# Kernel tuning notes

Measured on AMD Instinct MI355X. Metric: run time of the kernel, lower is better.

Reference implementation:

```python
import jax, jax.numpy as jnp
import numpy as np

MAX_SIGMA = 10.0
TRUNCATE = 4.0
R = int(TRUNCATE * MAX_SIGMA + 0.5)  # 40, static max radius (scipy: int(truncate*sigma+0.5))
L = 2 * R + 1                         # 81


def _make_kernels(sigmas):
    # sigmas: [B] -> kernels [B, L], exactly matching scipy._gaussian_kernel1d
    pos = jnp.arange(-R, R + 1, dtype=sigmas.dtype)          # [L]
    r = jnp.floor(TRUNCATE * sigmas + 0.5)                   # per-sample radius
    w = jnp.exp(-0.5 * (pos[None, :] ** 2) / (sigmas[:, None] ** 2))
    w = w * (jnp.abs(pos)[None, :] <= r[:, None])            # scipy truncation
    return w / jnp.sum(w, axis=-1, keepdims=True)


def _reflect_index(n):
    # symmetric ('reflect' in scipy) boundary indices for pad width R, valid even if R > n
    i = jnp.arange(-R, n + R)
    j = jnp.mod(i, 2 * n)
    return jnp.where(j < n, j, 2 * n - 1 - j)


def _conv_last(x, k):
    # correlate along last axis with reflect boundary; x [..., n], k [L]
    n = x.shape[-1]
    xp = x[..., _reflect_index(n)]                            # [..., n+2R]
    flat = xp.reshape(-1, 1, n + 2 * R)
    out = jax.lax.conv_general_dilated(flat, k[None, None, :],
                                       window_strides=(1,), padding='VALID')
    return out.reshape(x.shape)


def _blur_one(xi, k):
    # xi: [C, H, W]; scipy gaussian_filter with scalar sigma blurs every axis
    for ax in range(xi.ndim):
        xi = jnp.moveaxis(_conv_last(jnp.moveaxis(xi, ax, -1), k), -1, ax)
    return xi


def setup_inputs() -> dict:
    key = jax.random.key(0)
    k1, _ = jax.random.split(key)
    B, C, H, W = 64, 3, 512, 512
    x = jax.random.uniform(k1, (B, C, H, W), dtype=jnp.float32)
    blur_sigmas = jnp.asarray(np.geomspace(0.5, MAX_SIGMA, 10), dtype=jnp.float32)
    fwd_steps = jax.random.randint(jax.random.fold_in(key, 1), (B,), 0, 10, dtype=jnp.int32)
    return {"x": x, "blur_sigmas": blur_sigmas, "fwd_steps": fwd_steps}


def reference(x, blur_sigmas, fwd_steps):
    sigmas = blur_sigmas[fwd_steps]          # [B]
    kernels = _make_kernels(sigmas)          # [B, L]
    return jax.vmap(_blur_one)(x, kernels)   # [B, C, H, W]
```

## Files before the change

kernel.cpp:

```cpp
#include <hip/hip_runtime.h>
#include <hip/hip_bf16.h>

#define RMAX 40
#define LK   81
#define HH   512
#define WW   512
#define CC   3
#define BB   64
#define ROWS 2

__global__ void prep_kernel(const float* __restrict__ sigmas10,
                            const int* __restrict__ steps,
                            int* __restrict__ rbuf,
                            float* __restrict__ mbuf,
                            float* __restrict__ wbuf)
{
    int b = threadIdx.x;
    if (b >= BB) return;
    float sigma = sigmas10[steps[b]];
    int r = (int)floorf(4.0f * sigma + 0.5f);
    if (r > RMAX) r = RMAX;
    float s2 = sigma * sigma;

    float sum = 0.0f;
    for (int p = -r; p <= r; ++p)
        sum += expf(-0.5f * (float)(p * p) / s2);
    float inv = 1.0f / sum;

    for (int i = 0; i < 128; ++i) wbuf[b * 128 + i] = 0.0f;
    for (int p = -r; p <= r; ++p)
        wbuf[b * 128 + 16 + (p + RMAX)] = expf(-0.5f * (float)(p * p) / s2) * inv;

    float Mm[9];
    for (int i = 0; i < 9; ++i) Mm[i] = 0.0f;
    for (int p = -r; p <= r; ++p) {
        float wv = expf(-0.5f * (float)(p * p) / s2) * inv;
        for (int c = 0; c < CC; ++c) {
            int i = c + p;
            int j = ((i % 6) + 6) % 6;
            int cc = (j < 3) ? j : 5 - j;
            Mm[c * 3 + cc] += wv;
        }
    }
    for (int c = 0; c < 3; ++c)
        for (int cc = 0; cc < 3; ++cc)
            mbuf[b * 12 + c * 4 + cc] = Mm[c * 3 + cc];
    rbuf[b] = r;
}

__global__ __launch_bounds__(256) void passB_kernel(
    const float* __restrict__ x,
    const float* __restrict__ wbuf,
    const float* __restrict__ mbuf,
    const int*   __restrict__ rbuf,
    float* __restrict__ out1)
{
    __shared__ __align__(16) float mixed[CC * ROWS][WW + 2 * RMAX];

    const int b   = blockIdx.y;
    const int h0  = blockIdx.x * ROWS;
    const int tid = threadIdx.x;
    const int r   = __builtin_amdgcn_readfirstlane(rbuf[b]);

    const float M00 = mbuf[b * 12 + 0], M01 = mbuf[b * 12 + 1], M02 = mbuf[b * 12 + 2];
    const float M10 = mbuf[b * 12 + 4], M11 = mbuf[b * 12 + 5], M12 = mbuf[b * 12 + 6];
    const float M20 = mbuf[b * 12 + 8], M21 = mbuf[b * 12 + 9], M22 = mbuf[b * 12 + 10];

    const float* xb = x + (size_t)b * CC * HH * WW + (size_t)h0 * WW;

    for (int idx = tid; idx < WW + 2 * RMAX; idx += 256) {
        int i  = idx - RMAX;
        int jm = i & (2 * WW - 1);
        int src = (jm < WW) ? jm : (2 * WW - 1 - jm);
        float a0 = __builtin_nontemporal_load(xb + src);
        float a1 = __builtin_nontemporal_load(xb + HH * WW + src);
        float a2 = __builtin_nontemporal_load(xb + 2 * HH * WW + src);
        float b0 = __builtin_nontemporal_load(xb + WW + src);
        float b1 = __builtin_nontemporal_load(xb + HH * WW + WW + src);
        float b2 = __builtin_nontemporal_load(xb + 2 * HH * WW + WW + src);
        mixed[0][idx] = M00 * a0 + M01 * a1 + M02 * a2;
        mixed[1][idx] = M00 * b0 + M01 * b1 + M02 * b2;
        mixed[2][idx] = M10 * a0 + M11 * a1 + M12 * a2;
        mixed[3][idx] = M10 * b0 + M11 * b1 + M12 * b2;
        mixed[4][idx] = M20 * a0 + M21 * a1 + M22 * a2;
        mixed[5][idx] = M20 * b0 + M21 * b1 + M22 * b2;
    }
    __syncthreads();

    const int t0    = (RMAX - r) & ~3;
    const int n4    = ((r + RMAX + 3 - t0) >> 2) + 1;
    const int kbase = (16 + t0) >> 2;
    const float4* K4 = (const float4*)(wbuf + b * 128);

#pragma unroll
    for (int k = 0; k < 3; ++k) {
        const int task = tid + 256 * k;
        const int g    = task & 127;
        const int rc   = task >> 7;
        const int w0   = g << 2;

        const int dbase = (w0 + t0) >> 2;
        const float4* D4 = (const float4*)(&mixed[rc][0]);

        float4 Wlo = K4[kbase - 1];
        float acc0 = 0.f, acc1 = 0.f, acc2 = 0.f, acc3 = 0.f;

        for (int s = 0; s < n4; ++s) {
            float4 Whi = K4[kbase + s];
            float4 D   = D4[dbase + s];
            acc0 += Whi.x * D.x; acc1 += Wlo.w * D.x; acc2 += Wlo.z * D.x; acc3 += Wlo.y * D.x;
            acc0 += Whi.y * D.y; acc1 += Whi.x * D.y; acc2 += Wlo.w * D.y; acc3 += Wlo.z * D.y;
            acc0 += Whi.z * D.z; acc1 += Whi.y * D.z; acc2 += Whi.x * D.z; acc3 += Wlo.w * D.z;
            acc0 += Whi.w * D.w; acc1 += Whi.z * D.w; acc2 += Whi.y * D.w; acc3 += Whi.x * D.w;
            Wlo = Whi;
        }

        float4 o; o.x = acc0; o.y = acc1; o.z = acc2; o.w = acc3;
        const int c = rc >> 1, row = rc & 1;
        float* dst = out1 + ((size_t)b * CC + c) * HH * WW
                   + (size_t)(h0 + row) * WW + w0;
        *(float4*)dst = o;
    }
}

__device__ __forceinline__ int refl512(int i) {
    int jm = i & (2 * HH - 1);
    return (jm < HH) ? jm : (2 * HH - 1 - jm);
}

__global__ __launch_bounds__(256) void passC_kernel(
    const float* __restrict__ in1,
    const float* __restrict__ wbuf,
    const int*   __restrict__ rbuf,
    float* __restrict__ out)
{
    const int tid = threadIdx.x;
    const int w   = blockIdx.x * 256 + tid;
    const int h0  = blockIdx.y * 16;
    const int bc  = blockIdx.z;
    const int b   = bc / 3;
    const int r   = __builtin_amdgcn_readfirstlane(rbuf[b]);

    const float* src = in1 + (size_t)bc * HH * WW;
    const float* kw  = wbuf + b * 128;

    float acc[16];
    float D[16];
#pragma unroll
    for (int j = 0; j < 16; ++j) acc[j] = 0.0f;

#pragma unroll
    for (int q = 0; q < 16; ++q)
        D[q] = src[(size_t)refl512(h0 - r + q) * WW + w];

    const int Mr = (2 * r + 16) & ~15;

    for (int c0 = 0; c0 < Mr; c0 += 16) {
#pragma unroll
        for (int u = 0; u < 16; ++u) {
            int m = c0 + u;
            float wgt = kw[16 + RMAX - r + m];
#pragma unroll
            for (int j = 0; j < 16; ++j)
                acc[j] += wgt * D[(u + j) & 15];
            D[u] = src[(size_t)refl512(h0 - r + m + 16) * WW + w];
        }
    }

    float* dst = out + (size_t)bc * HH * WW + (size_t)h0 * WW + w;
#pragma unroll
    for (int j = 0; j < 16; ++j)
        __builtin_nontemporal_store(acc[j], dst + (size_t)j * WW);
}

extern "C" void kernel_launch(void* const* d_in, const int* in_sizes, int n_in,
                              void* d_out, int out_size, void* d_ws, size_t ws_size,
                              hipStream_t stream)
{
    const float* x      = (const float*)d_in[0];
    const float* sigmas = (const float*)d_in[1];
    const int*   steps  = (const int*)d_in[2];
    float*       out    = (float*)d_out;

    int*   rbuf  = (int*)d_ws;
    float* mbuf  = (float*)((char*)d_ws + 256);
    float* wbuf  = (float*)((char*)d_ws + 4096);
    float* inter = (float*)((char*)d_ws + 65536);

    prep_kernel<<<1, 64, 0, stream>>>(sigmas, steps, rbuf, mbuf, wbuf);

    dim3 gB(HH / ROWS, BB);
    passB_kernel<<<gB, 256, 0, stream>>>(x, wbuf, mbuf, rbuf, inter);

    dim3 gC(WW / 256, HH / 16, BB * CC);
    passC_kernel<<<gC, 256, 0, stream>>>(inter, wbuf, rbuf, out);
}
```

Measured before the change: 469.6 us.

## Store intermediate blur in bf16 and enlarge vertical pass tile to 32 rows

The horizontal pass now writes its intermediate result as bf16 instead of fp32, halving intermediate write and read traffic. The vertical pass reads bf16 and converts to float, and each thread now computes 32 output rows instead of 16, which cuts the redundant halo reads per output. Costs are lost precision in the intermediate (bf16 rounding may break tolerance) and higher register pressure from 32-entry accumulator and data arrays.

New measurement: 423.1 us. 1.11x faster.

```diff
diff --git a/kernel.cpp b/kernel.cpp
--- a/kernel.cpp
+++ b/kernel.cpp
@@ -8,6 +8,18 @@
 #define CC   3
 #define BB   64
 #define ROWS 2
+#define TH   32
+
+typedef unsigned short u16;
+
+__device__ __forceinline__ u16 f2bf(float f) {
+    unsigned u = __float_as_uint(f);
+    u += 0x7FFFu + ((u >> 16) & 1u);
+    return (u16)(u >> 16);
+}
+__device__ __forceinline__ float bf2f(u16 s) {
+    return __uint_as_float(((unsigned)s) << 16);
+}
 
 __global__ void prep_kernel(const float* __restrict__ sigmas10,
                             const int* __restrict__ steps,
@@ -53,7 +65,7 @@
     const float* __restrict__ wbuf,
     const float* __restrict__ mbuf,
     const int*   __restrict__ rbuf,
-    float* __restrict__ out1)
+    u16* __restrict__ out1)
 {
     __shared__ __align__(16) float mixed[CC * ROWS][WW + 2 * RMAX];
 
@@ -115,11 +127,12 @@
             Wlo = Whi;
         }
 
-        float4 o; o.x = acc0; o.y = acc1; o.z = acc2; o.w = acc3;
+        ushort4 o;
+        o.x = f2bf(acc0); o.y = f2bf(acc1); o.z = f2bf(acc2); o.w = f2bf(acc3);
         const int c = rc >> 1, row = rc & 1;
-        float* dst = out1 + ((size_t)b * CC + c) * HH * WW
-                   + (size_t)(h0 + row) * WW + w0;
-        *(float4*)dst = o;
+        u16* dst = out1 + ((size_t)b * CC + c) * HH * WW
+                 + (size_t)(h0 + row) * WW + w0;
+        *(ushort4*)dst = o;
     }
 }
 
@@ -129,47 +142,47 @@
 }
 
 __global__ __launch_bounds__(256) void passC_kernel(
-    const float* __restrict__ in1,
+    const u16* __restrict__ in1,
     const float* __restrict__ wbuf,
     const int*   __restrict__ rbuf,
     float* __restrict__ out)
 {
     const int tid = threadIdx.x;
     const int w   = blockIdx.x * 256 + tid;
-    const int h0  = blockIdx.y * 16;
+    const int h0  = blockIdx.y * TH;
     const int bc  = blockIdx.z;
     const int b   = bc / 3;
     const int r   = __builtin_amdgcn_readfirstlane(rbuf[b]);
 
-    const float* src = in1 + (size_t)bc * HH * WW;
+    const u16*  src = in1 + (size_t)bc * HH * WW;
     const float* kw  = wbuf + b * 128;
 
-    float acc[16];
-    float D[16];
-#pragma unroll
-    for (int j = 0; j < 16; ++j) acc[j] = 0.0f;
-
-#pragma unroll
-    for (int q = 0; q < 16; ++q)
-        D[q] = src[(size_t)refl512(h0 - r + q) * WW + w];
-
-    const int Mr = (2 * r + 16) & ~15;
-
-    for (int c0 = 0; c0 < Mr; c0 += 16) {
-#pragma unroll
-        for (int u = 0; u < 16; ++u) {
+    float acc[TH];
+    float D[TH];
+#pragma unroll
+    for (int j = 0; j < TH; ++j) acc[j] = 0.0f;
+
+#pragma unroll
+    for (int q = 0; q < TH; ++q)
+        D[q] = bf2f(src[(size_t)refl512(h0 - r + q) * WW + w]);
+
+    const int Mr = (2 * r + TH) & ~(TH - 1);
+
+    for (int c0 = 0; c0 < Mr; c0 += TH) {
+#pragma unroll
+        for (int u = 0; u < TH; ++u) {
             int m = c0 + u;
             float wgt = kw[16 + RMAX - r + m];
 #pragma unroll
-            for (int j = 0; j < 16; ++j)
-                acc[j] += wgt * D[(u + j) & 15];
-            D[u] = src[(size_t)refl512(h0 - r + m + 16) * WW + w];
+            for (int j = 0; j < TH; ++j)
+                acc[j] += wgt * D[(u + j) & (TH - 1)];
+            D[u] = bf2f(src[(size_t)refl512(h0 - r + m + TH) * WW + w]);
         }
     }
 
     float* dst = out + (size_t)bc * HH * WW + (size_t)h0 * WW + w;
 #pragma unroll
-    for (int j = 0; j < 16; ++j)
+    for (int j = 0; j < TH; ++j)
         __builtin_nontemporal_store(acc[j], dst + (size_t)j * WW);
 }
 
@@ -185,13 +198,13 @@
     int*   rbuf  = (int*)d_ws;
     float* mbuf  = (float*)((char*)d_ws + 256);
     float* wbuf  = (float*)((char*)d_ws + 4096);
-    float* inter = (float*)((char*)d_ws + 65536);
+    u16*   inter = (u16*)((char*)d_ws + 65536);
 
     prep_kernel<<<1, 64, 0, stream>>>(sigmas, steps, rbuf, mbuf, wbuf);
 
     dim3 gB(HH / ROWS, BB);
     passB_kernel<<<gB, 256, 0, stream>>>(x, wbuf, mbuf, rbuf, inter);
 
-    dim3 gC(WW / 256, HH / 16, BB * CC);
+    dim3 gC(WW / 256, HH / TH, BB * CC);
     passC_kernel<<<gC, 256, 0, stream>>>(inter, wbuf, rbuf, out);
 }
```
